# Optimization experiments

Measured on AMD Instinct MI355X. Metric: run time of the kernel, lower is better.

## Reference

```python
import jax, jax.numpy as jnp
import numpy as np

MIN_CURV = 1e-06
MIN_NORM = 1e-15

def _norm(x):
    return jnp.clip(jnp.linalg.norm(x, axis=-1, keepdims=True), MIN_NORM, None)

def lorentz_expmap0(v, c):
    sqrt_c = jnp.sqrt(c)
    vn = _norm(v)
    x0 = jnp.cosh(sqrt_c * vn) / sqrt_c
    xs = jnp.sinh(sqrt_c * vn) * v / (sqrt_c * vn)
    return jnp.concatenate([x0, xs], axis=-1)

def lorentz_logmap0(x, c):
    sqrt_c = jnp.sqrt(c)
    x0 = x[..., 0:1]
    xs = x[..., 1:]
    xs_norm = _norm(xs)
    theta = jnp.arccosh(jnp.clip(sqrt_c * x0, 1.0 + 1e-07, None))
    return theta / (sqrt_c * xs_norm) * xs

def lorentz_project(x, c):
    spatial = x[..., 1:]
    sq = jnp.sum(spatial * spatial, axis=-1, keepdims=True)
    x0 = jnp.clip(jnp.sqrt(sq + 1.0 / c), MIN_NORM, None)
    return jnp.concatenate([x0, spatial], axis=-1)

def givens_rotation(x, angles):
    x0 = x[..., 0:1]
    xs = x[..., 1:]
    cos_a = jnp.cos(angles)
    sin_a = jnp.sin(angles)
    xe = xs[..., 0::2]
    xo = xs[..., 1::2]
    ne = cos_a * xe - sin_a * xo
    no = sin_a * xe + cos_a * xo
    xr = jnp.stack([ne, no], axis=-1).reshape(xs.shape)
    return jnp.concatenate([x0, xr], axis=-1)

def setup_inputs() -> dict:
    key = jax.random.key(0)
    ks = jax.random.split(key, 16)
    N_NODE, E, B = 50000, 500000, 64
    IN_DIM, OUT_DIM, ATTN_DIM, N_REL = 128, 128, 128, 200
    N_EMB = 2 * N_REL + 1  # 401
    hidden = jax.random.normal(ks[0], (N_NODE, IN_DIM), dtype=jnp.float32)
    q_sub = jax.random.randint(ks[1], (B,), 0, N_NODE)
    q_rel = jax.random.randint(ks[2], (B,), 0, N_EMB)
    r_idx = jax.random.randint(ks[3], (E,), 0, B)
    rel = jax.random.randint(ks[4], (E,), 0, N_EMB)
    sub = jax.random.randint(ks[5], (E,), 0, N_NODE)
    obj = jax.random.randint(ks[6], (E,), 0, N_NODE)
    zeros = jnp.zeros((E,), dtype=jnp.int32)
    edges = jnp.stack([r_idx, zeros, rel, zeros, sub, obj], axis=1)
    rela_embed = jax.random.normal(ks[7], (N_EMB, IN_DIM), dtype=jnp.float32)
    rel_angles = jax.random.uniform(ks[8], (N_EMB, IN_DIM // 2), minval=-0.1, maxval=0.1, dtype=jnp.float32)
    curvature = jnp.array(1.0, dtype=jnp.float32)
    Ws_w = jax.random.normal(ks[9], (ATTN_DIM, IN_DIM), dtype=jnp.float32) * 0.05
    Wr_w = jax.random.normal(ks[10], (ATTN_DIM, IN_DIM), dtype=jnp.float32) * 0.05
    Wqr_w = jax.random.normal(ks[11], (ATTN_DIM, IN_DIM), dtype=jnp.float32) * 0.05
    Wqr_b = jax.random.normal(ks[12], (ATTN_DIM,), dtype=jnp.float32) * 0.05
    Wattn_w = jax.random.normal(ks[13], (1, ATTN_DIM), dtype=jnp.float32) * 0.05
    Wh_w = jax.random.normal(ks[14], (OUT_DIM, IN_DIM), dtype=jnp.float32) * 0.05
    return {"hidden": hidden, "rela_embed": rela_embed, "rel_angles": rel_angles,
            "curvature": curvature, "Ws_w": Ws_w, "Wr_w": Wr_w, "Wqr_w": Wqr_w,
            "Wqr_b": Wqr_b, "Wattn_w": Wattn_w, "Wh_w": Wh_w,
            "q_sub": q_sub, "q_rel": q_rel, "edges": edges,
            "n_node": N_NODE, "old_nodes_new_idx": jnp.arange(N_NODE)}

def reference(hidden, rela_embed, rel_angles, curvature, Ws_w, Wr_w, Wqr_w, Wqr_b,
              Wattn_w, Wh_w, q_sub, q_rel, edges, n_node, old_nodes_new_idx):
    sub = edges[:, 4]
    rel = edges[:, 2]
    obj = edges[:, 5]
    r_idx = edges[:, 0]
    hs = hidden[sub]                      # [E, in_dim]
    hr = rela_embed[rel]                  # [E, in_dim]
    h_qr = rela_embed[q_rel][r_idx]       # [E, in_dim]
    pre = jax.nn.relu(hs @ Ws_w.T + hr @ Wr_w.T + h_qr @ Wqr_w.T + Wqr_b)
    alpha = jax.nn.sigmoid(pre @ Wattn_w.T)  # [E, 1]
    c = jnp.clip(curvature, MIN_CURV, None)
    mess_tangent = hs + hr
    mess_L = lorentz_expmap0(mess_tangent, c)          # [E, in_dim+1]
    mess_L = givens_rotation(mess_L, rel_angles[rel])
    mess2 = lorentz_logmap0(mess_L, c)                 # [E, in_dim]
    message = mess2 * alpha
    message_agg = jax.ops.segment_sum(message, obj, num_segments=n_node)
    a = message_agg @ Wh_w.T                           # [n_node, out_dim]
    a_L = lorentz_expmap0(a, c)
    # act is identity; project back to hyperboloid and log-map
    a_L = lorentz_project(jnp.concatenate([a_L[..., 0:1], a_L[..., 1:]], axis=-1), c)
    hidden_new = lorentz_logmap0(a_L, c)
    return hidden_new
```

## Files before the change

kernel.cpp:

```cpp
#include <hip/hip_runtime.h>
#include <math.h>

#define D 128
#define CAP 36

typedef _Float16 f16x8 __attribute__((ext_vector_type(8)));
typedef _Float16 f16x4 __attribute__((ext_vector_type(4)));
typedef _Float16 f16x2 __attribute__((ext_vector_type(2)));
typedef float    f32x4 __attribute__((ext_vector_type(4)));

union H8 { f16x8 v; f16x4 q[2]; f16x2 p[4]; _Float16 f[8]; };
union H4 { f16x4 v; f16x2 p[2]; _Float16 f[4]; };

__device__ __forceinline__ float fdot2f(f16x2 a, f16x2 b, float c){
  return __builtin_amdgcn_fdot2(a, b, c, false);
}
__device__ __forceinline__ f16x2 relu2(f16x2 x){
  f16x2 r;
  r[0] = x[0] > (_Float16)0 ? x[0] : (_Float16)0;
  r[1] = x[1] > (_Float16)0 ? x[1] : (_Float16)0;
  return r;
}
__device__ __forceinline__ float rsum32(float v){
  v += __shfl_xor(v, 16);
  v += __shfl_xor(v, 8);
  v += __shfl_xor(v, 4);
  v += __shfl_xor(v, 2);
  v += __shfl_xor(v, 1);
  return v;
}


__device__ __forceinline__ void hgemm_core16(const _Float16* __restrict__ A,
                                             const _Float16* __restrict__ W,
                                             int arow, f32x4 acc[8], int quad, int lo){
  #pragma unroll
  for (int kt=0;kt<4;kt++){
    f16x8 a = *(const f16x8*)(A + (size_t)arow*D + kt*32 + quad*8);
    #pragma unroll
    for (int nt=0;nt<8;nt++){
      f16x8 b = *(const f16x8*)(W + (size_t)(nt*16 + lo)*D + kt*32 + quad*8);
      acc[nt] = __builtin_amdgcn_mfma_f32_16x16x32_f16(a, b, acc[nt], 0, 0, 0);
    }
  }
}

__device__ __forceinline__ void store_wpart(_Float16* __restrict__ O, f32x4 acc[8],
                                            int m0, int quad, int lo, int M){
  int r0 = m0 + quad*4;
  #pragma unroll
  for (int i=0;i<4;i++){
    int r = r0 + i;
    if (r < M){
      H4 s1, s2;
      #pragma unroll
      for (int nt=0;nt<4;nt++){
        s1.f[nt] = (_Float16)acc[nt][i];
        s2.f[nt] = (_Float16)acc[nt+4][i];
      }
      *(f16x4*)(O + (size_t)r*256 + lo*16 + 4)  = s1.v;
      *(f16x4*)(O + (size_t)r*256 + lo*16 + 12) = s2.v;
    }
  }
}

__global__ __launch_bounds__(256) void k_prep(
    const float* __restrict__ rela, const float* __restrict__ rel_angles,
    const float* __restrict__ Ws, const float* __restrict__ Wr,
    const float* __restrict__ Wh, const float* __restrict__ Wqr,
    const float* __restrict__ Wqr_b, const int* __restrict__ q_rel,
    _Float16* __restrict__ rela16, _Float16* __restrict__ relhq,
    _Float16* __restrict__ relcs, _Float16* __restrict__ Ws16,
    _Float16* __restrict__ Wr16, _Float16* __restrict__ Wh16,
    _Float16* __restrict__ hqw16, int* __restrict__ cnt,
    int NEMB, int NN, int PA){
  __shared__ float emb[D];
  int b = blockIdx.x;
  int t = threadIdx.x;
  if (b < PA){
    int idx = b*256 + t;
    int T1 = NEMB*32;
    if (idx < T1){
      int r = idx >> 5, l = idx & 31;
      float4 hv = *(const float4*)(rela + (size_t)r*D + l*4);
      f16x4 h = { (_Float16)hv.x, (_Float16)hv.y, (_Float16)hv.z, (_Float16)hv.w };
      *(f16x4*)(rela16 + (size_t)r*D + l*4) = h;
      *(f16x4*)(relhq  + (size_t)r*256 + l*8) = h;
      float2 an = *(const float2*)(rel_angles + (size_t)r*(D/2) + l*2);
      float c0 = cosf(an.x), s0 = sinf(an.x);
      float c1 = cosf(an.y), s1 = sinf(an.y);
      H8 cs;
      cs.f[0]=(_Float16)c0; cs.f[1]=(_Float16)(-s0); cs.f[2]=(_Float16)s0; cs.f[3]=(_Float16)c0;
      cs.f[4]=(_Float16)c1; cs.f[5]=(_Float16)(-s1); cs.f[6]=(_Float16)s1; cs.f[7]=(_Float16)c1;
      *(f16x8*)(relcs + (size_t)r*256 + l*8) = cs.v;
      return;
    }
    int j = idx - T1;
    if (j < 3*D*D/4){
      const float* src = (j < 4096) ? Ws : (j < 8192) ? Wr : Wh;
      _Float16*    dst = (j < 4096) ? Ws16 : (j < 8192) ? Wr16 : Wh16;
      int o = (j & 4095)*4;
      float4 v = *(const float4*)(src + o);
      f16x4 h = { (_Float16)v.x, (_Float16)v.y, (_Float16)v.z, (_Float16)v.w };
      *(f16x4*)(dst + o) = h;
      return;
    }
    j -= 3*D*D/4;
    if (j < NN) cnt[j] = 0;
  } else {
    int bb = b - PA;
    if (t < D) emb[t] = rela[(size_t)q_rel[bb]*D + t];
    __syncthreads();
    if (t < D){
      float acc = Wqr_b[t];
      #pragma unroll 8
      for (int k=0;k<D;k++) acc += emb[k]*Wqr[t*D + k];
      int p = ((t & 15) << 3) + (t >> 4);
      hqw16[bb*D + p] = (_Float16)acc;
    }
  }
}

__global__ __launch_bounds__(256) void k_mega(
    const int* __restrict__ edges, int* __restrict__ cnt, int* __restrict__ bucket,
    int E, const float* __restrict__ hidden, const _Float16* __restrict__ Ws16,
    _Float16* __restrict__ hw16, int NN,
    const _Float16* __restrict__ rela16, const _Float16* __restrict__ Wr16,
    _Float16* __restrict__ relhq, int NEMB, int SB, int GH){
  int b = blockIdx.x;
  if (b < SB){
    int e0 = (b*256 + threadIdx.x)*4;
    if (e0 >= E) return;
    if (e0 + 3 < E){
      const int4* q = (const int4*)(edges + (size_t)e0*6);
      int4 q0=q[0], q1=q[1], q2=q[2], q3=q[3], q4=q[4], q5=q[5];
      int key0 = q1.x | (q0.z << 17) | (q0.x << 26);
      int key1 = q2.z | (q2.x << 17) | (q1.z << 26);
      int key2 = q4.x | (q3.z << 17) | (q3.x << 26);
      int key3 = q5.z | (q5.x << 17) | (q4.z << 26);
      int p0 = atomicAdd(cnt + q1.y, 1);
      int p1 = atomicAdd(cnt + q2.w, 1);
      int p2 = atomicAdd(cnt + q4.y, 1);
      int p3 = atomicAdd(cnt + q5.w, 1);
      if (p0 < CAP) bucket[q1.y*CAP + p0] = key0;
      if (p1 < CAP) bucket[q2.w*CAP + p1] = key1;
      if (p2 < CAP) bucket[q4.y*CAP + p2] = key2;
      if (p3 < CAP) bucket[q5.w*CAP + p3] = key3;
    } else {
      for (int u=0; u<4; u++){
        int e = e0 + u;
        if (e < E){
          const int* er = edges + (size_t)e*6;
          int key = er[4] | (er[2] << 17) | (er[0] << 26);
          int pos = atomicAdd(cnt + er[5], 1);
          if (pos < CAP) bucket[er[5]*CAP + pos] = key;
        }
      }
    }
  } else if (b < SB + GH){
    int bb = b - SB;
    int wave = threadIdx.x >> 6;
    int lane = threadIdx.x & 63;
    int quad = lane >> 4, lo = lane & 15;
    int m0 = bb*64 + wave*16;
    int arow = min(m0 + lo, NN-1);
    f32x4 acc[8];
    #pragma unroll
    for (int nt=0;nt<8;nt++) acc[nt] = (f32x4){0.f,0.f,0.f,0.f};
    H8 hpack[4];
    #pragma unroll
    for (int kt=0;kt<4;kt++){
      float4 a0 = *(const float4*)(hidden + (size_t)arow*D + kt*32 + quad*8);
      float4 a1 = *(const float4*)(hidden + (size_t)arow*D + kt*32 + quad*8 + 4);
      H8 a;
      a.f[0]=(_Float16)a0.x; a.f[1]=(_Float16)a0.y; a.f[2]=(_Float16)a0.z; a.f[3]=(_Float16)a0.w;
      a.f[4]=(_Float16)a1.x; a.f[5]=(_Float16)a1.y; a.f[6]=(_Float16)a1.z; a.f[7]=(_Float16)a1.w;
      hpack[kt] = a;
      #pragma unroll
      for (int nt=0;nt<8;nt++){
        f16x8 bb2 = *(const f16x8*)(Ws16 + (size_t)(nt*16 + lo)*D + kt*32 + quad*8);
        acc[nt] = __builtin_amdgcn_mfma_f32_16x16x32_f16(a.v, bb2, acc[nt], 0, 0, 0);
      }
    }
    if (m0 + lo < NN){
      #pragma unroll
      for (int kt=0;kt<4;kt++){
        int g = kt*8 + quad*2;
        *(f16x4*)(hw16 + (size_t)arow*256 + g*8)     = hpack[kt].q[0];
        *(f16x4*)(hw16 + (size_t)arow*256 + (g+1)*8) = hpack[kt].q[1];
      }
    }
    store_wpart(hw16, acc, m0, quad, lo, NN);
  } else {
    int bb = b - SB - GH;
    int wave = threadIdx.x >> 6;
    int lane = threadIdx.x & 63;
    int quad = lane >> 4, lo = lane & 15;
    int m0 = bb*64 + wave*16;
    int arow = min(m0 + lo, NEMB-1);
    f32x4 acc[8];
    #pragma unroll
    for (int nt=0;nt<8;nt++) acc[nt] = (f32x4){0.f,0.f,0.f,0.f};
    hgemm_core16(rela16, Wr16, arow, acc, quad, lo);
    store_wpart(relhq, acc, m0, quad, lo, NEMB);
  }
}

__device__ __forceinline__ void edge_op(int key,
    const _Float16* __restrict__ hw16, const _Float16* __restrict__ relcs,
    const _Float16* __restrict__ relhq, const _Float16* __restrict__ hqw16,
    unsigned lh8, unsigned lh4, f16x2 wa01, f16x2 wa23,
    float& ax, float& ay, float& az, float& aw){
  unsigned sub = key & 0x1FFFF, rel = ((unsigned)key >> 17) & 0x1FF, ri = (unsigned)key >> 26;
  H8 hw; hw.v = *(const f16x8*)(hw16  + (sub << 8) + lh8);
  H8 cs; cs.v = *(const f16x8*)(relcs + (rel << 8) + lh8);
  H8 hq; hq.v = *(const f16x8*)(relhq + (rel << 8) + lh8);
  H4 qw; qw.v = *(const f16x4*)(hqw16 + (ri  << 7) + lh4);
  f16x2 t01 = relu2(hw.p[2] + hq.p[2] + qw.p[0]);
  f16x2 t23 = relu2(hw.p[3] + hq.p[3] + qw.p[1]);
  float s = fdot2f(t01, wa01, fdot2f(t23, wa23, 0.f));
  s = rsum32(s);
  float al = __builtin_amdgcn_rcpf(1.f + __expf(-s));
  f16x2 v01 = hw.p[0] + hq.p[0];
  f16x2 v23 = hw.p[1] + hq.p[1];
  ax += al * fdot2f(cs.p[0], v01, 0.f);
  ay += al * fdot2f(cs.p[1], v01, 0.f);
  az += al * fdot2f(cs.p[2], v23, 0.f);
  aw += al * fdot2f(cs.p[3], v23, 0.f);
}

__global__ __launch_bounds__(256) void k_aggregate(
    const _Float16* __restrict__ hw16, const _Float16* __restrict__ relcs,
    const _Float16* __restrict__ relhq, const _Float16* __restrict__ hqw16,
    const float* __restrict__ Wattn, const int* __restrict__ cnt,
    const int* __restrict__ bucket, _Float16* __restrict__ agg16, int NN){
  int t = threadIdx.x;
  int half = t >> 5, l = t & 31;
  int n = blockIdx.x*8 + half;
  if (n >= NN) return;
  unsigned lh8 = (unsigned)l*8, lh4 = (unsigned)l*4;
  unsigned p0 = (unsigned)l*4;
  float w0 = Wattn[(((p0+0)&7)<<4) + ((p0+0)>>3)];
  float w1 = Wattn[(((p0+1)&7)<<4) + ((p0+1)>>3)];
  float w2 = Wattn[(((p0+2)&7)<<4) + ((p0+2)>>3)];
  float w3 = Wattn[(((p0+3)&7)<<4) + ((p0+3)>>3)];
  f16x2 wa01 = { (_Float16)w0, (_Float16)w1 };
  f16x2 wa23 = { (_Float16)w2, (_Float16)w3 };

  int deg = min(cnt[n], CAP);
  const int* bk = bucket + n*CAP;
  float ax=0.f, ay=0.f, az=0.f, aw=0.f;

  int i = 0;
  for (; i+4 <= deg; i += 4){
    int4 q = *(const int4*)(bk + i);
    edge_op(q.x, hw16, relcs, relhq, hqw16, lh8, lh4, wa01, wa23, ax, ay, az, aw);
    edge_op(q.y, hw16, relcs, relhq, hqw16, lh8, lh4, wa01, wa23, ax, ay, az, aw);
    edge_op(q.z, hw16, relcs, relhq, hqw16, lh8, lh4, wa01, wa23, ax, ay, az, aw);
    edge_op(q.w, hw16, relcs, relhq, hqw16, lh8, lh4, wa01, wa23, ax, ay, az, aw);
  }
  for (; i < deg; i++)
    edge_op(bk[i], hw16, relcs, relhq, hqw16, lh8, lh4, wa01, wa23, ax, ay, az, aw);

  f16x4 o = { (_Float16)ax, (_Float16)ay, (_Float16)az, (_Float16)aw };
  *(f16x4*)(agg16 + ((size_t)n << 7) + lh4) = o;
}

__global__ __launch_bounds__(256) void k_hgemm0(const _Float16* __restrict__ A,
                                                const _Float16* __restrict__ W,
                                                float* __restrict__ O, int M){
  int wave = threadIdx.x >> 6;
  int lane = threadIdx.x & 63;
  int quad = lane >> 4, lo = lane & 15;
  int m0 = blockIdx.x*64 + wave*16;
  int arow = min(m0 + lo, M-1);
  f32x4 acc[8];
  #pragma unroll
  for (int nt=0;nt<8;nt++) acc[nt] = (f32x4){0.f,0.f,0.f,0.f};
  hgemm_core16(A, W, arow, acc, quad, lo);
  int r0 = m0 + quad*4;
  #pragma unroll
  for (int nt=0;nt<8;nt++){
    int c = nt*16 + lo;
    #pragma unroll
    for (int i=0;i<4;i++){
      int r = r0 + i;
      if (r < M) O[(size_t)r*D + c] = acc[nt][i];
    }
  }
}

extern "C" void kernel_launch(void* const* d_in, const int* in_sizes, int n_in,
                              void* d_out, int out_size, void* d_ws, size_t ws_size,
                              hipStream_t stream){
  const float* hidden     = (const float*)d_in[0];
  const float* rela       = (const float*)d_in[1];
  const float* rel_angles = (const float*)d_in[2];
  const float* Ws         = (const float*)d_in[4];
  const float* Wr         = (const float*)d_in[5];
  const float* Wqr        = (const float*)d_in[6];
  const float* Wqr_b      = (const float*)d_in[7];
  const float* Wattn      = (const float*)d_in[8];
  const float* Wh         = (const float*)d_in[9];
  const int*   q_rel      = (const int*)d_in[11];
  const int*   edges      = (const int*)d_in[12];

  int NN   = in_sizes[0] / D;
  int NEMB = in_sizes[1] / D;
  int B    = in_sizes[11];
  int E    = in_sizes[12] / 6;

  char* p = (char*)d_ws;
  auto alloc = [&](size_t bytes)->char*{
    char* r = p; p += (bytes + 255) & ~(size_t)255; return r;
  };
  _Float16* hw16   = (_Float16*)alloc((size_t)NN*256*2);
  _Float16* agg16  = (_Float16*)alloc((size_t)NN*D*2);
  _Float16* rela16 = (_Float16*)alloc((size_t)NEMB*D*2);
  _Float16* relhq  = (_Float16*)alloc((size_t)NEMB*256*2);
  _Float16* relcs  = (_Float16*)alloc((size_t)NEMB*256*2);
  _Float16* hqw16  = (_Float16*)alloc((size_t)B*D*2);
  _Float16* Ws16   = (_Float16*)alloc((size_t)D*D*2);
  _Float16* Wr16   = (_Float16*)alloc((size_t)D*D*2);
  _Float16* Wh16   = (_Float16*)alloc((size_t)D*D*2);
  int*      cnt    = (int*)alloc((size_t)NN*4);
  int*      bucket = (int*)alloc((size_t)NN*CAP*4);

  int smallN = NEMB*32 + 3*D*D/4 + NN;
  int PA = (smallN + 255)/256;
  k_prep<<<PA + B, 256, 0, stream>>>(rela, rel_angles, Ws, Wr, Wh, Wqr, Wqr_b,
                                     q_rel, rela16, relhq, relcs, Ws16, Wr16,
                                     Wh16, hqw16, cnt, NEMB, NN, PA);

  int SB = (E + 1023)/1024;
  int GH = (NN + 63)/64;
  int G1 = (NEMB + 63)/64;
  k_mega<<<SB + GH + G1, 256, 0, stream>>>(edges, cnt, bucket, E, hidden, Ws16,
                                           hw16, NN, rela16, Wr16, relhq, NEMB,
                                           SB, GH);

  k_aggregate<<<(NN+7)/8, 256, 0, stream>>>(hw16, relcs, relhq, hqw16,
                                            Wattn, cnt, bucket, agg16, NN);
  k_hgemm0<<<(NN+63)/64, 256, 0, stream>>>(agg16, Wh16, (float*)d_out, NN);
}
```

Before: 241.7 us.

## Software-pipeline hidden-row gathers and batch attention reductions across four edges

The aggregation kernel now prefetches the next group of four edges' hidden rows while it processes the current group, using a double-buffered loop. It also merges the four per-edge attention score reductions into a single butterfly shuffle sequence, so each lane reduces one edge's score and the resulting alphas are redistributed. Launch bounds add a minimum of 4 blocks per SM. These changes aim to hide gather latency and cut shuffle count, at the cost of higher register pressure, which the occupancy hint may turn into spills.

After: 237.1 us. Within noise of the previous version (-1.9%).

```diff
diff --git a/kernel.cpp b/kernel.cpp
--- a/kernel.cpp
+++ b/kernel.cpp
@@ -229,7 +229,81 @@
   aw += al * fdot2f(cs.p[3], v23, 0.f);
 }
 
-__global__ __launch_bounds__(256) void k_aggregate(
+__device__ __forceinline__ void group4(
+    int4 q, const H8& h0, const H8& h1, const H8& h2, const H8& h3,
+    const _Float16* __restrict__ relcs, const _Float16* __restrict__ relhq,
+    const _Float16* __restrict__ hqw16,
+    unsigned lh8, unsigned lh4, int l, f16x2 wa01, f16x2 wa23,
+    float& ax, float& ay, float& az, float& aw){
+  unsigned r0 = ((unsigned)q.x >> 17) & 0x1FF, i0 = (unsigned)q.x >> 26;
+  unsigned r1 = ((unsigned)q.y >> 17) & 0x1FF, i1 = (unsigned)q.y >> 26;
+  unsigned r2 = ((unsigned)q.z >> 17) & 0x1FF, i2 = (unsigned)q.z >> 26;
+  unsigned r3 = ((unsigned)q.w >> 17) & 0x1FF, i3 = (unsigned)q.w >> 26;
+  H8 c0,c1,c2,c3, e0,e1,e2,e3; H4 w0,w1,w2,w3;
+  c0.v = *(const f16x8*)(relcs + (r0 << 8) + lh8);
+  c1.v = *(const f16x8*)(relcs + (r1 << 8) + lh8);
+  c2.v = *(const f16x8*)(relcs + (r2 << 8) + lh8);
+  c3.v = *(const f16x8*)(relcs + (r3 << 8) + lh8);
+  e0.v = *(const f16x8*)(relhq + (r0 << 8) + lh8);
+  e1.v = *(const f16x8*)(relhq + (r1 << 8) + lh8);
+  e2.v = *(const f16x8*)(relhq + (r2 << 8) + lh8);
+  e3.v = *(const f16x8*)(relhq + (r3 << 8) + lh8);
+  w0.v = *(const f16x4*)(hqw16 + (i0 << 7) + lh4);
+  w1.v = *(const f16x4*)(hqw16 + (i1 << 7) + lh4);
+  w2.v = *(const f16x4*)(hqw16 + (i2 << 7) + lh4);
+  w3.v = *(const f16x4*)(hqw16 + (i3 << 7) + lh4);
+  f16x2 ta, tb;
+  ta = relu2(h0.p[2] + e0.p[2] + w0.p[0]); tb = relu2(h0.p[3] + e0.p[3] + w0.p[1]);
+  float s0 = fdot2f(ta, wa01, fdot2f(tb, wa23, 0.f));
+  ta = relu2(h1.p[2] + e1.p[2] + w1.p[0]); tb = relu2(h1.p[3] + e1.p[3] + w1.p[1]);
+  float s1 = fdot2f(ta, wa01, fdot2f(tb, wa23, 0.f));
+  ta = relu2(h2.p[2] + e2.p[2] + w2.p[0]); tb = relu2(h2.p[3] + e2.p[3] + w2.p[1]);
+  float s2 = fdot2f(ta, wa01, fdot2f(tb, wa23, 0.f));
+  ta = relu2(h3.p[2] + e3.p[2] + w3.p[0]); tb = relu2(h3.p[3] + e3.p[3] + w3.p[1]);
+  float s3 = fdot2f(ta, wa01, fdot2f(tb, wa23, 0.f));
+  bool b0 = (l & 1) != 0, b1 = (l & 2) != 0;
+  float x01 = b0 ? s1 : s0, y01 = b0 ? s0 : s1;
+  float r01 = x01 + __shfl_xor(y01, 1);
+  float x23 = b0 ? s3 : s2, y23 = b0 ? s2 : s3;
+  float r23 = x23 + __shfl_xor(y23, 1);
+  float xa = b1 ? r23 : r01, ya = b1 ? r01 : r23;
+  float rr = xa + __shfl_xor(ya, 2);
+  rr += __shfl_xor(rr, 4);
+  rr += __shfl_xor(rr, 8);
+  rr += __shfl_xor(rr, 16);
+  float av = __builtin_amdgcn_rcpf(1.f + __expf(-rr));
+  float aB = __shfl_xor(av, 1);
+  float aC = __shfl_xor(av, 2);
+  float aD = __shfl_xor(aB, 2);
+  float g0 = b0 ? aB : av, g1 = b0 ? av : aB, g2 = b0 ? aD : aC, g3 = b0 ? aC : aD;
+  float al0 = b1 ? g2 : g0, al1 = b1 ? g3 : g1, al2 = b1 ? g0 : g2, al3 = b1 ? g1 : g3;
+  f16x2 v01, v23;
+  v01 = h0.p[0] + e0.p[0]; v23 = h0.p[1] + e0.p[1];
+  float dx0 = fdot2f(c0.p[0], v01, 0.f), dy0 = fdot2f(c0.p[1], v01, 0.f);
+  float dz0 = fdot2f(c0.p[2], v23, 0.f), dw0 = fdot2f(c0.p[3], v23, 0.f);
+  v01 = h1.p[0] + e1.p[0]; v23 = h1.p[1] + e1.p[1];
+  float dx1 = fdot2f(c1.p[0], v01, 0.f), dy1 = fdot2f(c1.p[1], v01, 0.f);
+  float dz1 = fdot2f(c1.p[2], v23, 0.f), dw1 = fdot2f(c1.p[3], v23, 0.f);
+  v01 = h2.p[0] + e2.p[0]; v23 = h2.p[1] + e2.p[1];
+  float dx2 = fdot2f(c2.p[0], v01, 0.f), dy2 = fdot2f(c2.p[1], v01, 0.f);
+  float dz2 = fdot2f(c2.p[2], v23, 0.f), dw2 = fdot2f(c2.p[3], v23, 0.f);
+  v01 = h3.p[0] + e3.p[0]; v23 = h3.p[1] + e3.p[1];
+  float dx3 = fdot2f(c3.p[0], v01, 0.f), dy3 = fdot2f(c3.p[1], v01, 0.f);
+  float dz3 = fdot2f(c3.p[2], v23, 0.f), dw3 = fdot2f(c3.p[3], v23, 0.f);
+  ax += al0*dx0 + al1*dx1 + al2*dx2 + al3*dx3;
+  ay += al0*dy0 + al1*dy1 + al2*dy2 + al3*dy3;
+  az += al0*dz0 + al1*dz1 + al2*dz2 + al3*dz3;
+  aw += al0*dw0 + al1*dw1 + al2*dw2 + al3*dw3;
+}
+
+#define HWLOAD(Q, H0,H1,H2,H3) do{ \
+  H0.v = *(const f16x8*)(hw16 + ((((unsigned)(Q).x) & 0x1FFFF) << 8) + lh8); \
+  H1.v = *(const f16x8*)(hw16 + ((((unsigned)(Q).y) & 0x1FFFF) << 8) + lh8); \
+  H2.v = *(const f16x8*)(hw16 + ((((unsigned)(Q).z) & 0x1FFFF) << 8) + lh8); \
+  H3.v = *(const f16x8*)(hw16 + ((((unsigned)(Q).w) & 0x1FFFF) << 8) + lh8); \
+}while(0)
+
+__global__ __launch_bounds__(256, 4) void k_aggregate(
     const _Float16* __restrict__ hw16, const _Float16* __restrict__ relcs,
     const _Float16* __restrict__ relhq, const _Float16* __restrict__ hqw16,
     const float* __restrict__ Wattn, const int* __restrict__ cnt,
@@ -251,13 +325,22 @@
   const int* bk = bucket + n*CAP;
   float ax=0.f, ay=0.f, az=0.f, aw=0.f;
 
-  int i = 0;
-  for (; i+4 <= deg; i += 4){
-    int4 q = *(const int4*)(bk + i);
-    edge_op(q.x, hw16, relcs, relhq, hqw16, lh8, lh4, wa01, wa23, ax, ay, az, aw);
-    edge_op(q.y, hw16, relcs, relhq, hqw16, lh8, lh4, wa01, wa23, ax, ay, az, aw);
-    edge_op(q.z, hw16, relcs, relhq, hqw16, lh8, lh4, wa01, wa23, ax, ay, az, aw);
-    edge_op(q.w, hw16, relcs, relhq, hqw16, lh8, lh4, wa01, wa23, ax, ay, az, aw);
+  int nb = deg >> 2;
+  int i = nb << 2;
+  if (nb){
+    int4 qA = *(const int4*)bk;
+    int4 qB;
+    H8 a0,a1,a2,a3, b0h,b1h,b2h,b3h;
+    HWLOAD(qA, a0,a1,a2,a3);
+    int g = 0;
+    for (;;){
+      if (g+1 < nb){ qB = *(const int4*)(bk + g*4 + 4); HWLOAD(qB, b0h,b1h,b2h,b3h); }
+      group4(qA, a0,a1,a2,a3, relcs, relhq, hqw16, lh8, lh4, l, wa01, wa23, ax, ay, az, aw);
+      if (++g >= nb) break;
+      if (g+1 < nb){ qA = *(const int4*)(bk + g*4 + 4); HWLOAD(qA, a0,a1,a2,a3); }
+      group4(qB, b0h,b1h,b2h,b3h, relcs, relhq, hqw16, lh8, lh4, l, wa01, wa23, ax, ay, az, aw);
+      if (++g >= nb) break;
+    }
   }
   for (; i < deg; i++)
     edge_op(bk[i], hw16, relcs, relhq, hqw16, lh8, lh4, wa01, wa23, ax, ay, az, aw);
```

## Software-pipeline aggregate gathers in groups of four with batched attention reductions

Applied to the files above, without the earlier changes.

The edge aggregation loop now loads gathered rows for four edges at once, double-buffered so the next group's loads are issued before the current group is computed. The four per-edge attention logit reductions are merged into one butterfly that transposes partial sums across lanes, cutting cross-lane shuffles per edge, and tail edges are masked instead of handled by a scalar loop. It also sets a minimum occupancy hint of three blocks. The two register buffers raise register pressure, which may cap occupancy or cause spills, and masked tail edges load row 0 needlessly.

New measurement: 253.2 us. +4.8%, slower.

```diff
diff --git a/kernel.cpp b/kernel.cpp
--- a/kernel.cpp
+++ b/kernel.cpp
@@ -20,14 +20,6 @@
   r[0] = x[0] > (_Float16)0 ? x[0] : (_Float16)0;
   r[1] = x[1] > (_Float16)0 ? x[1] : (_Float16)0;
   return r;
-}
-__device__ __forceinline__ float rsum32(float v){
-  v += __shfl_xor(v, 16);
-  v += __shfl_xor(v, 8);
-  v += __shfl_xor(v, 4);
-  v += __shfl_xor(v, 2);
-  v += __shfl_xor(v, 1);
-  return v;
 }
 
 
@@ -206,30 +198,97 @@
   }
 }
 
-__device__ __forceinline__ void edge_op(int key,
+struct G {
+  H8 h0,h1,h2,h3;
+  H8 c0,c1,c2,c3;
+  H8 e0,e1,e2,e3;
+  H4 w0,w1,w2,w3;
+  float m1,m2,m3;
+};
+
+__device__ __forceinline__ void gload(const int* __restrict__ bk, int g, int deg,
     const _Float16* __restrict__ hw16, const _Float16* __restrict__ relcs,
     const _Float16* __restrict__ relhq, const _Float16* __restrict__ hqw16,
-    unsigned lh8, unsigned lh4, f16x2 wa01, f16x2 wa23,
+    unsigned lh8, unsigned lh4, G& o){
+  int4 q = *(const int4*)(bk + (g << 2));
+  int base = g << 2;
+  bool v1 = base + 1 < deg, v2 = base + 2 < deg, v3 = base + 3 < deg;
+  if (!v1) q.y = 0;
+  if (!v2) q.z = 0;
+  if (!v3) q.w = 0;
+  o.m1 = v1 ? 1.f : 0.f;
+  o.m2 = v2 ? 1.f : 0.f;
+  o.m3 = v3 ? 1.f : 0.f;
+  unsigned s0 = (unsigned)q.x & 0x1FFFF, r0 = ((unsigned)q.x >> 17) & 0x1FF, i0 = (unsigned)q.x >> 26;
+  unsigned s1 = (unsigned)q.y & 0x1FFFF, r1 = ((unsigned)q.y >> 17) & 0x1FF, i1 = (unsigned)q.y >> 26;
+  unsigned s2 = (unsigned)q.z & 0x1FFFF, r2 = ((unsigned)q.z >> 17) & 0x1FF, i2 = (unsigned)q.z >> 26;
+  unsigned s3 = (unsigned)q.w & 0x1FFFF, r3 = ((unsigned)q.w >> 17) & 0x1FF, i3 = (unsigned)q.w >> 26;
+  o.h0.v = *(const f16x8*)(hw16 + (s0 << 8) + lh8);
+  o.h1.v = *(const f16x8*)(hw16 + (s1 << 8) + lh8);
+  o.h2.v = *(const f16x8*)(hw16 + (s2 << 8) + lh8);
+  o.h3.v = *(const f16x8*)(hw16 + (s3 << 8) + lh8);
+  o.c0.v = *(const f16x8*)(relcs + (r0 << 8) + lh8);
+  o.c1.v = *(const f16x8*)(relcs + (r1 << 8) + lh8);
+  o.c2.v = *(const f16x8*)(relcs + (r2 << 8) + lh8);
+  o.c3.v = *(const f16x8*)(relcs + (r3 << 8) + lh8);
+  o.e0.v = *(const f16x8*)(relhq + (r0 << 8) + lh8);
+  o.e1.v = *(const f16x8*)(relhq + (r1 << 8) + lh8);
+  o.e2.v = *(const f16x8*)(relhq + (r2 << 8) + lh8);
+  o.e3.v = *(const f16x8*)(relhq + (r3 << 8) + lh8);
+  o.w0.v = *(const f16x4*)(hqw16 + (i0 << 7) + lh4);
+  o.w1.v = *(const f16x4*)(hqw16 + (i1 << 7) + lh4);
+  o.w2.v = *(const f16x4*)(hqw16 + (i2 << 7) + lh4);
+  o.w3.v = *(const f16x4*)(hqw16 + (i3 << 7) + lh4);
+}
+
+__device__ __forceinline__ void gcompute(const G& A, int l, f16x2 wa01, f16x2 wa23,
     float& ax, float& ay, float& az, float& aw){
-  unsigned sub = key & 0x1FFFF, rel = ((unsigned)key >> 17) & 0x1FF, ri = (unsigned)key >> 26;
-  H8 hw; hw.v = *(const f16x8*)(hw16  + (sub << 8) + lh8);
-  H8 cs; cs.v = *(const f16x8*)(relcs + (rel << 8) + lh8);
-  H8 hq; hq.v = *(const f16x8*)(relhq + (rel << 8) + lh8);
-  H4 qw; qw.v = *(const f16x4*)(hqw16 + (ri  << 7) + lh4);
-  f16x2 t01 = relu2(hw.p[2] + hq.p[2] + qw.p[0]);
-  f16x2 t23 = relu2(hw.p[3] + hq.p[3] + qw.p[1]);
-  float s = fdot2f(t01, wa01, fdot2f(t23, wa23, 0.f));
-  s = rsum32(s);
-  float al = __builtin_amdgcn_rcpf(1.f + __expf(-s));
-  f16x2 v01 = hw.p[0] + hq.p[0];
-  f16x2 v23 = hw.p[1] + hq.p[1];
-  ax += al * fdot2f(cs.p[0], v01, 0.f);
-  ay += al * fdot2f(cs.p[1], v01, 0.f);
-  az += al * fdot2f(cs.p[2], v23, 0.f);
-  aw += al * fdot2f(cs.p[3], v23, 0.f);
-}
-
-__global__ __launch_bounds__(256) void k_aggregate(
+  f16x2 ta, tb;
+  ta = relu2(A.h0.p[2] + A.e0.p[2] + A.w0.p[0]); tb = relu2(A.h0.p[3] + A.e0.p[3] + A.w0.p[1]);
+  float s0 = fdot2f(ta, wa01, fdot2f(tb, wa23, 0.f));
+  ta = relu2(A.h1.p[2] + A.e1.p[2] + A.w1.p[0]); tb = relu2(A.h1.p[3] + A.e1.p[3] + A.w1.p[1]);
+  float s1 = fdot2f(ta, wa01, fdot2f(tb, wa23, 0.f));
+  ta = relu2(A.h2.p[2] + A.e2.p[2] + A.w2.p[0]); tb = relu2(A.h2.p[3] + A.e2.p[3] + A.w2.p[1]);
+  float s2 = fdot2f(ta, wa01, fdot2f(tb, wa23, 0.f));
+  ta = relu2(A.h3.p[2] + A.e3.p[2] + A.w3.p[0]); tb = relu2(A.h3.p[3] + A.e3.p[3] + A.w3.p[1]);
+  float s3 = fdot2f(ta, wa01, fdot2f(tb, wa23, 0.f));
+  bool b0 = (l & 1) != 0, b1 = (l & 2) != 0;
+  float x01 = b0 ? s1 : s0, y01 = b0 ? s0 : s1;
+  float r01 = x01 + __shfl_xor(y01, 1);
+  float x23 = b0 ? s3 : s2, y23 = b0 ? s2 : s3;
+  float r23 = x23 + __shfl_xor(y23, 1);
+  float xa = b1 ? r23 : r01, ya = b1 ? r01 : r23;
+  float rr = xa + __shfl_xor(ya, 2);
+  rr += __shfl_xor(rr, 4);
+  rr += __shfl_xor(rr, 8);
+  rr += __shfl_xor(rr, 16);
+  float av = __builtin_amdgcn_rcpf(1.f + __expf(-rr));
+  float aB = __shfl_xor(av, 1);
+  float aC = __shfl_xor(av, 2);
+  float aD = __shfl_xor(aB, 2);
+  float g0 = b0 ? aB : av, g1 = b0 ? av : aB, g2 = b0 ? aD : aC, g3 = b0 ? aC : aD;
+  float al0 = b1 ? g2 : g0, al1 = b1 ? g3 : g1, al2 = b1 ? g0 : g2, al3 = b1 ? g1 : g3;
+  al1 *= A.m1; al2 *= A.m2; al3 *= A.m3;
+  f16x2 v01, v23;
+  v01 = A.h0.p[0] + A.e0.p[0]; v23 = A.h0.p[1] + A.e0.p[1];
+  float dx0 = fdot2f(A.c0.p[0], v01, 0.f), dy0 = fdot2f(A.c0.p[1], v01, 0.f);
+  float dz0 = fdot2f(A.c0.p[2], v23, 0.f), dw0 = fdot2f(A.c0.p[3], v23, 0.f);
+  v01 = A.h1.p[0] + A.e1.p[0]; v23 = A.h1.p[1] + A.e1.p[1];
+  float dx1 = fdot2f(A.c1.p[0], v01, 0.f), dy1 = fdot2f(A.c1.p[1], v01, 0.f);
+  float dz1 = fdot2f(A.c1.p[2], v23, 0.f), dw1 = fdot2f(A.c1.p[3], v23, 0.f);
+  v01 = A.h2.p[0] + A.e2.p[0]; v23 = A.h2.p[1] + A.e2.p[1];
+  float dx2 = fdot2f(A.c2.p[0], v01, 0.f), dy2 = fdot2f(A.c2.p[1], v01, 0.f);
+  float dz2 = fdot2f(A.c2.p[2], v23, 0.f), dw2 = fdot2f(A.c2.p[3], v23, 0.f);
+  v01 = A.h3.p[0] + A.e3.p[0]; v23 = A.h3.p[1] + A.e3.p[1];
+  float dx3 = fdot2f(A.c3.p[0], v01, 0.f), dy3 = fdot2f(A.c3.p[1], v01, 0.f);
+  float dz3 = fdot2f(A.c3.p[2], v23, 0.f), dw3 = fdot2f(A.c3.p[3], v23, 0.f);
+  ax += al0*dx0 + al1*dx1 + al2*dx2 + al3*dx3;
+  ay += al0*dy0 + al1*dy1 + al2*dy2 + al3*dy3;
+  az += al0*dz0 + al1*dz1 + al2*dz2 + al3*dz3;
+  aw += al0*dw0 + al1*dw1 + al2*dw2 + al3*dw3;
+}
+
+__global__ __launch_bounds__(256, 3) void k_aggregate(
     const _Float16* __restrict__ hw16, const _Float16* __restrict__ relcs,
     const _Float16* __restrict__ relhq, const _Float16* __restrict__ hqw16,
     const float* __restrict__ Wattn, const int* __restrict__ cnt,
@@ -251,16 +310,20 @@
   const int* bk = bucket + n*CAP;
   float ax=0.f, ay=0.f, az=0.f, aw=0.f;
 
-  int i = 0;
-  for (; i+4 <= deg; i += 4){
-    int4 q = *(const int4*)(bk + i);
-    edge_op(q.x, hw16, relcs, relhq, hqw16, lh8, lh4, wa01, wa23, ax, ay, az, aw);
-    edge_op(q.y, hw16, relcs, relhq, hqw16, lh8, lh4, wa01, wa23, ax, ay, az, aw);
-    edge_op(q.z, hw16, relcs, relhq, hqw16, lh8, lh4, wa01, wa23, ax, ay, az, aw);
-    edge_op(q.w, hw16, relcs, relhq, hqw16, lh8, lh4, wa01, wa23, ax, ay, az, aw);
-  }
-  for (; i < deg; i++)
-    edge_op(bk[i], hw16, relcs, relhq, hqw16, lh8, lh4, wa01, wa23, ax, ay, az, aw);
+  int ng = (deg + 3) >> 2;
+  if (ng){
+    G A, B;
+    gload(bk, 0, deg, hw16, relcs, relhq, hqw16, lh8, lh4, A);
+    int g = 0;
+    for (;;){
+      if (g + 1 < ng) gload(bk, g+1, deg, hw16, relcs, relhq, hqw16, lh8, lh4, B);
+      gcompute(A, l, wa01, wa23, ax, ay, az, aw);
+      if (++g >= ng) break;
+      if (g + 1 < ng) gload(bk, g+1, deg, hw16, relcs, relhq, hqw16, lh8, lh4, A);
+      gcompute(B, l, wa01, wa23, ax, ay, az, aw);
+      if (++g >= ng) break;
+    }
+  }
 
   f16x4 o = { (_Float16)ax, (_Float16)ay, (_Float16)az, (_Float16)aw };
   *(f16x4*)(agg16 + ((size_t)n << 7) + lh4) = o;
```
